# Optimization experiments

Hardware: AMD Instinct MI355X
Metric: run time of the kernel (lower is better)

The kernel has to match this reference:

```python
import jax, jax.numpy as jnp
import numpy as np

# loss weights from LineSegmentLoss.loss_w_dict (defaults)
W_TP_CENTER = 10.0

def smooth_l1(pred, gt):
    # F.smooth_l1_loss with default beta=1.0, reduction='none'
    d = jnp.abs(pred - gt)
    return jnp.where(d < 1.0, 0.5 * d * d, d - 0.5)

def bce_with_logits(logits, targets):
    # numerically stable BCE-with-logits, elementwise
    return jnp.maximum(logits, 0.0) - logits * targets + jnp.log1p(jnp.exp(-jnp.abs(logits)))

def weighted_bce_with_logits(out, gt, pos_w, neg_w):
    pos_mask = (gt != 0).astype(out.dtype)
    neg_mask = 1.0 - pos_mask
    loss = bce_with_logits(out, gt)
    loss_pos = (loss * pos_mask).sum() / pos_mask.sum()
    loss_neg = (loss * neg_mask).sum() / neg_mask.sum()
    return loss_pos * pos_w + loss_neg * neg_w

def displacement_loss_func(pred_dis, gt_dis):
    # pred_dis, gt_dis: [B, 4, H, W]
    pos_v = jnp.abs(gt_dis).sum(axis=1)                      # [B,H,W]
    pos_mask = (pos_v != 0).astype(pred_dis.dtype)           # [B,H,W]
    pos_mask_sum = pos_mask.sum()
    m = pos_mask[:, None, :, :]
    pred_m = pred_dis * m
    gt_m = gt_dis * m
    loss1 = smooth_l1(pred_m, gt_m).sum(axis=1)              # [B,H,W]
    # swap endpoints (x0,y0,x1,y1) -> (x1,y1,x0,y0)
    pred_swap = jnp.concatenate([pred_m[:, 2:], pred_m[:, :2]], axis=1)
    loss2 = smooth_l1(pred_swap, gt_m).sum(axis=1)
    return jnp.minimum(loss1, loss2).sum() / pos_mask_sum

def len_and_angle_loss_func(pred_len, pred_angle, gt_len, gt_angle):
    pred_len = jax.nn.sigmoid(pred_len)
    pred_angle = jax.nn.sigmoid(pred_angle)
    pos_mask = (gt_len != 0).astype(pred_len.dtype)
    pos_mask_sum = pos_mask.sum()
    len_loss = (smooth_l1(pred_len, gt_len) * pos_mask).sum() / pos_mask_sum
    angle_loss = (smooth_l1(pred_angle, gt_angle) * pos_mask).sum() / pos_mask_sum
    return len_loss, angle_loss

def setup_inputs() -> dict:
    key = jax.random.key(0)
    k1, k2, k3, k4, k5 = jax.random.split(key, 5)
    B, C, H, W = 32, 16, 256, 256
    preds = jax.random.normal(k1, (B, C, H, W), dtype=jnp.float32)
    base = jax.random.uniform(k2, (B, C, H, W), dtype=jnp.float32)
    keep = (jax.random.uniform(k3, (B, 1, H, W)) < 0.05).astype(jnp.float32)
    gts = base * keep
    tp_lines = jax.random.uniform(k4, (B, 64, 4), dtype=jnp.float32) * 512.0
    sol_lines = jax.random.uniform(k5, (B, 64, 4), dtype=jnp.float32) * 512.0
    return {"preds": preds, "gts": gts,
            "tp_gt_lines_512_list": tp_lines,
            "sol_gt_lines_512_list": sol_lines}

def reference(preds, gts, tp_gt_lines_512_list, sol_gt_lines_512_list):
    # line / junction segmentation losses (ch 15, 14)
    line_seg_loss = weighted_bce_with_logits(preds[:, 15], gts[:, 15], 1.0, 1.0)
    junc_seg_loss = weighted_bce_with_logits(preds[:, 14], gts[:, 14], 1.0, 30.0)
    # SOL block (ch 0..6)
    sol_center = weighted_bce_with_logits(preds[:, 0], gts[:, 0], 1.0, 30.0)
    sol_disp = displacement_loss_func(preds[:, 1:5], gts[:, 1:5])
    sol_len, sol_angle = len_and_angle_loss_func(preds[:, 5], preds[:, 6], gts[:, 5], gts[:, 6])
    # TP block (ch 7..13)
    tp_center = weighted_bce_with_logits(preds[:, 7], gts[:, 7], 1.0, 30.0)
    tp_disp = displacement_loss_func(preds[:, 8:12], gts[:, 8:12])
    tp_len, tp_angle = len_and_angle_loss_func(preds[:, 12], preds[:, 13], gts[:, 12], gts[:, 13])
    total = (W_TP_CENTER * tp_center + tp_disp + tp_len + tp_angle
             + sol_center + sol_disp + sol_len + sol_angle
             + line_seg_loss + junc_seg_loss)
    return total
```

## Files before the change

kernel.cpp:

```cpp
#include <hip/hip_runtime.h>
#include <math.h>

#define HW 65536
#define HW4 16384
#define CTOT 16
#define BATCH 32
#define NPIX (BATCH * HW)
#define NGRP (NPIX / 4)

#define NACC 22

__device__ __forceinline__ float smooth_l1(float p, float g) {
    float d = fabsf(p - g);
    return (d < 1.0f) ? 0.5f * d * d : d - 0.5f;
}
__device__ __forceinline__ float bce_logits(float x, float t) {
    return fmaxf(x, 0.0f) - x * t + log1pf(expf(-fabsf(x)));
}
__device__ __forceinline__ float sigmoidf_(float x) {
    return 1.0f / (1.0f + expf(-x));
}
__device__ __forceinline__ float get4(const float4& v, int j) {
    return j == 0 ? v.x : (j == 1 ? v.y : (j == 2 ? v.z : v.w));
}

__global__ __launch_bounds__(256) void loss_kernel(const float* __restrict__ preds,
                                                   const float* __restrict__ gts,
                                                   double* __restrict__ ws) {
    float acc[NACC];
#pragma unroll
    for (int i = 0; i < NACC; ++i) acc[i] = 0.0f;

    const int gtid = blockIdx.x * blockDim.x + threadIdx.x;
    const int stride = gridDim.x * blockDim.x;

    for (int g = gtid; g < NGRP; g += stride) {
        const int b   = g >> 14;
        const int hw4 = g & (HW4 - 1);
        const float4* pb = (const float4*)preds + (size_t)b * (CTOT * HW4) + hw4;
        const float4* gb = (const float4*)gts   + (size_t)b * (CTOT * HW4) + hw4;

        {
            const int ch[4]   = {15, 14, 0, 7};
            const int base[4] = {0, 3, 6, 9};
#pragma unroll
            for (int k = 0; k < 4; ++k) {
                float4 p = pb[(size_t)ch[k] * HW4];
                float4 t = gb[(size_t)ch[k] * HW4];
#pragma unroll
                for (int j = 0; j < 4; ++j) {
                    float x  = get4(p, j);
                    float tv = get4(t, j);
                    float loss = bce_logits(x, tv);
                    float pos  = (tv != 0.0f) ? 1.0f : 0.0f;
                    acc[base[k] + 0] += loss * pos;
                    acc[base[k] + 1] += loss * (1.0f - pos);
                    acc[base[k] + 2] += pos;
                }
            }
        }

        {
            const int c0[2]   = {1, 8};
            const int base[2] = {12, 14};
#pragma unroll
            for (int k = 0; k < 2; ++k) {
                float4 p0 = pb[(size_t)(c0[k] + 0) * HW4];
                float4 p1 = pb[(size_t)(c0[k] + 1) * HW4];
                float4 p2 = pb[(size_t)(c0[k] + 2) * HW4];
                float4 p3 = pb[(size_t)(c0[k] + 3) * HW4];
                float4 g0 = gb[(size_t)(c0[k] + 0) * HW4];
                float4 g1 = gb[(size_t)(c0[k] + 1) * HW4];
                float4 g2 = gb[(size_t)(c0[k] + 2) * HW4];
                float4 g3 = gb[(size_t)(c0[k] + 3) * HW4];
#pragma unroll
                for (int j = 0; j < 4; ++j) {
                    float a0 = get4(p0, j), a1 = get4(p1, j), a2 = get4(p2, j), a3 = get4(p3, j);
                    float b0 = get4(g0, j), b1 = get4(g1, j), b2 = get4(g2, j), b3 = get4(g3, j);
                    float posv = fabsf(b0) + fabsf(b1) + fabsf(b2) + fabsf(b3);
                    float m = (posv != 0.0f) ? 1.0f : 0.0f;
                    float l1 = smooth_l1(a0, b0) + smooth_l1(a1, b1) +
                               smooth_l1(a2, b2) + smooth_l1(a3, b3);
                    float l2 = smooth_l1(a2, b0) + smooth_l1(a3, b1) +
                               smooth_l1(a0, b2) + smooth_l1(a1, b3);
                    acc[base[k] + 0] += fminf(l1, l2) * m;
                    acc[base[k] + 1] += m;
                }
            }
        }

        {
            const int cl[2]   = {5, 12};
            const int base[2] = {16, 19};
#pragma unroll
            for (int k = 0; k < 2; ++k) {
                float4 pl = pb[(size_t)(cl[k] + 0) * HW4];
                float4 pa = pb[(size_t)(cl[k] + 1) * HW4];
                float4 gl = gb[(size_t)(cl[k] + 0) * HW4];
                float4 ga = gb[(size_t)(cl[k] + 1) * HW4];
#pragma unroll
                for (int j = 0; j < 4; ++j) {
                    float glv = get4(gl, j);
                    float m = (glv != 0.0f) ? 1.0f : 0.0f;
                    acc[base[k] + 0] += smooth_l1(sigmoidf_(get4(pl, j)), glv) * m;
                    acc[base[k] + 1] += smooth_l1(sigmoidf_(get4(pa, j)), get4(ga, j)) * m;
                    acc[base[k] + 2] += m;
                }
            }
        }
    }

#pragma unroll
    for (int i = 0; i < NACC; ++i) {
        float v = acc[i];
#pragma unroll
        for (int off = 32; off > 0; off >>= 1) v += __shfl_down(v, off, 64);
        acc[i] = v;
    }

    __shared__ float red[4][NACC];
    const int lane = threadIdx.x & 63;
    const int wid  = threadIdx.x >> 6;
    if (lane == 0) {
#pragma unroll
        for (int i = 0; i < NACC; ++i) red[wid][i] = acc[i];
    }
    __syncthreads();
    if (threadIdx.x < NACC) {
        float s = red[0][threadIdx.x] + red[1][threadIdx.x] +
                  red[2][threadIdx.x] + red[3][threadIdx.x];
        atomicAdd(&ws[threadIdx.x], (double)s);
    }
}

__global__ void finalize_kernel(const double* __restrict__ ws, float* __restrict__ out) {
    if (threadIdx.x == 0 && blockIdx.x == 0) {
        const double N = (double)NPIX;
        double line_seg   = ws[0] / ws[2]  +  1.0 * (ws[1]  / (N - ws[2]));
        double junc_seg   = ws[3] / ws[5]  + 30.0 * (ws[4]  / (N - ws[5]));
        double sol_center = ws[6] / ws[8]  + 30.0 * (ws[7]  / (N - ws[8]));
        double tp_center  = ws[9] / ws[11] + 30.0 * (ws[10] / (N - ws[11]));
        double sol_disp   = ws[12] / ws[13];
        double tp_disp    = ws[14] / ws[15];
        double sol_len    = ws[16] / ws[18];
        double sol_angle  = ws[17] / ws[18];
        double tp_len     = ws[19] / ws[21];
        double tp_angle   = ws[20] / ws[21];
        double total = 10.0 * tp_center + tp_disp + tp_len + tp_angle +
                       sol_center + sol_disp + sol_len + sol_angle +
                       line_seg + junc_seg;
        out[0] = (float)total;
    }
}

extern "C" void kernel_launch(void* const* d_in, const int* in_sizes, int n_in,
                              void* d_out, int out_size, void* d_ws, size_t ws_size,
                              hipStream_t stream) {
    const float* preds = (const float*)d_in[0];
    const float* gts   = (const float*)d_in[1];
    double* ws = (double*)d_ws;

    hipMemsetAsync(d_ws, 0, NACC * sizeof(double), stream);

    loss_kernel<<<1024, 256, 0, stream>>>(preds, gts, ws);
    finalize_kernel<<<1, 64, 0, stream>>>(ws, (float*)d_out);
}
```

Baseline: 297.4 us.

## Split loss kernel into per-task block ranges with fewer accumulators

Block indices are partitioned so each block handles a single loss term (BCE channel, displacement group, or len/angle pair) instead of every thread computing all 22 accumulators. This cuts register pressure and the reduction work per block, and doubles the grid to 2048 blocks. Load per block now varies: displacement blocks read 8 float4s per group while BCE blocks read 2, so block runtimes may be uneven and memory access is spread across different channel planes concurrently.

```diff
diff --git a/kernel.cpp b/kernel.cpp
--- a/kernel.cpp
+++ b/kernel.cpp
@@ -9,6 +9,8 @@
 #define NGRP (NPIX / 4)
 
 #define NACC 22
+
+#define GRID_BLOCKS 2048
 
 __device__ __forceinline__ float smooth_l1(float p, float g) {
     float d = fabsf(p - g);
@@ -27,109 +29,118 @@
 __global__ __launch_bounds__(256) void loss_kernel(const float* __restrict__ preds,
                                                    const float* __restrict__ gts,
                                                    double* __restrict__ ws) {
-    float acc[NACC];
+    const float4* pf = (const float4*)preds;
+    const float4* gf = (const float4*)gts;
+    const int blk = blockIdx.x;
+
+    float acc0 = 0.0f, acc1 = 0.0f, acc2 = 0.0f;
+    int base, nacc;
+
+    if (blk < 512) {
+        const int task = blk >> 7;
+        const int chs[4]   = {15, 14, 0, 7};
+        const int bases[4] = {0, 3, 6, 9};
+        const int ch = chs[task];
+        base = bases[task];
+        nacc = 3;
+        const int lthread = ((blk & 127) << 8) + threadIdx.x;
+        const int tstride = 128 * 256;
+#pragma unroll 2
+        for (int g = lthread; g < NGRP; g += tstride) {
+            const int b = g >> 14, hw4 = g & (HW4 - 1);
+            const size_t off = ((size_t)b * CTOT + ch) * HW4 + hw4;
+            float4 p = pf[off];
+            float4 t = gf[off];
 #pragma unroll
-    for (int i = 0; i < NACC; ++i) acc[i] = 0.0f;
-
-    const int gtid = blockIdx.x * blockDim.x + threadIdx.x;
-    const int stride = gridDim.x * blockDim.x;
-
-    for (int g = gtid; g < NGRP; g += stride) {
-        const int b   = g >> 14;
-        const int hw4 = g & (HW4 - 1);
-        const float4* pb = (const float4*)preds + (size_t)b * (CTOT * HW4) + hw4;
-        const float4* gb = (const float4*)gts   + (size_t)b * (CTOT * HW4) + hw4;
-
-        {
-            const int ch[4]   = {15, 14, 0, 7};
-            const int base[4] = {0, 3, 6, 9};
-#pragma unroll
-            for (int k = 0; k < 4; ++k) {
-                float4 p = pb[(size_t)ch[k] * HW4];
-                float4 t = gb[(size_t)ch[k] * HW4];
-#pragma unroll
-                for (int j = 0; j < 4; ++j) {
-                    float x  = get4(p, j);
-                    float tv = get4(t, j);
-                    float loss = bce_logits(x, tv);
-                    float pos  = (tv != 0.0f) ? 1.0f : 0.0f;
-                    acc[base[k] + 0] += loss * pos;
-                    acc[base[k] + 1] += loss * (1.0f - pos);
-                    acc[base[k] + 2] += pos;
-                }
+            for (int j = 0; j < 4; ++j) {
+                float x  = get4(p, j);
+                float tv = get4(t, j);
+                float loss = bce_logits(x, tv);
+                float pos  = (tv != 0.0f) ? 1.0f : 0.0f;
+                acc0 += loss * pos;
+                acc1 += loss * (1.0f - pos);
+                acc2 += pos;
             }
         }
-
-        {
-            const int c0[2]   = {1, 8};
-            const int base[2] = {12, 14};
+    } else if (blk < 1536) {
+        const int task = (blk - 512) >> 9;
+        const int c0 = task == 0 ? 1 : 8;
+        base = task == 0 ? 12 : 14;
+        nacc = 2;
+        const int lblk = (blk - 512) & 511;
+        const int lthread = (lblk << 8) + threadIdx.x;
+        const int tstride = 512 * 256;
+        for (int g = lthread; g < NGRP; g += tstride) {
+            const int b = g >> 14, hw4 = g & (HW4 - 1);
+            const size_t off = ((size_t)b * CTOT + c0) * HW4 + hw4;
+            float4 p0 = pf[off + 0 * HW4];
+            float4 p1 = pf[off + 1 * HW4];
+            float4 p2 = pf[off + 2 * HW4];
+            float4 p3 = pf[off + 3 * HW4];
+            float4 g0 = gf[off + 0 * HW4];
+            float4 g1 = gf[off + 1 * HW4];
+            float4 g2 = gf[off + 2 * HW4];
+            float4 g3 = gf[off + 3 * HW4];
 #pragma unroll
-            for (int k = 0; k < 2; ++k) {
-                float4 p0 = pb[(size_t)(c0[k] + 0) * HW4];
-                float4 p1 = pb[(size_t)(c0[k] + 1) * HW4];
-                float4 p2 = pb[(size_t)(c0[k] + 2) * HW4];
-                float4 p3 = pb[(size_t)(c0[k] + 3) * HW4];
-                float4 g0 = gb[(size_t)(c0[k] + 0) * HW4];
-                float4 g1 = gb[(size_t)(c0[k] + 1) * HW4];
-                float4 g2 = gb[(size_t)(c0[k] + 2) * HW4];
-                float4 g3 = gb[(size_t)(c0[k] + 3) * HW4];
-#pragma unroll
-                for (int j = 0; j < 4; ++j) {
-                    float a0 = get4(p0, j), a1 = get4(p1, j), a2 = get4(p2, j), a3 = get4(p3, j);
-                    float b0 = get4(g0, j), b1 = get4(g1, j), b2 = get4(g2, j), b3 = get4(g3, j);
-                    float posv = fabsf(b0) + fabsf(b1) + fabsf(b2) + fabsf(b3);
-                    float m = (posv != 0.0f) ? 1.0f : 0.0f;
-                    float l1 = smooth_l1(a0, b0) + smooth_l1(a1, b1) +
-                               smooth_l1(a2, b2) + smooth_l1(a3, b3);
-                    float l2 = smooth_l1(a2, b0) + smooth_l1(a3, b1) +
-                               smooth_l1(a0, b2) + smooth_l1(a1, b3);
-                    acc[base[k] + 0] += fminf(l1, l2) * m;
-                    acc[base[k] + 1] += m;
-                }
+            for (int j = 0; j < 4; ++j) {
+                float a0 = get4(p0, j), a1 = get4(p1, j), a2 = get4(p2, j), a3 = get4(p3, j);
+                float b0 = get4(g0, j), b1 = get4(g1, j), b2 = get4(g2, j), b3 = get4(g3, j);
+                float posv = fabsf(b0) + fabsf(b1) + fabsf(b2) + fabsf(b3);
+                float m = (posv != 0.0f) ? 1.0f : 0.0f;
+                float l1 = smooth_l1(a0, b0) + smooth_l1(a1, b1) +
+                           smooth_l1(a2, b2) + smooth_l1(a3, b3);
+                float l2 = smooth_l1(a2, b0) + smooth_l1(a3, b1) +
+                           smooth_l1(a0, b2) + smooth_l1(a1, b3);
+                acc0 += fminf(l1, l2) * m;
+                acc1 += m;
             }
         }
-
-        {
-            const int cl[2]   = {5, 12};
-            const int base[2] = {16, 19};
+    } else {
+        const int task = (blk - 1536) >> 8;
+        const int cl = task == 0 ? 5 : 12;
+        base = task == 0 ? 16 : 19;
+        nacc = 3;
+        const int lblk = (blk - 1536) & 255;
+        const int lthread = (lblk << 8) + threadIdx.x;
+        const int tstride = 256 * 256;
+#pragma unroll 2
+        for (int g = lthread; g < NGRP; g += tstride) {
+            const int b = g >> 14, hw4 = g & (HW4 - 1);
+            const size_t off = ((size_t)b * CTOT + cl) * HW4 + hw4;
+            float4 pl = pf[off + 0 * HW4];
+            float4 pa = pf[off + 1 * HW4];
+            float4 gl = gf[off + 0 * HW4];
+            float4 ga = gf[off + 1 * HW4];
 #pragma unroll
-            for (int k = 0; k < 2; ++k) {
-                float4 pl = pb[(size_t)(cl[k] + 0) * HW4];
-                float4 pa = pb[(size_t)(cl[k] + 1) * HW4];
-                float4 gl = gb[(size_t)(cl[k] + 0) * HW4];
-                float4 ga = gb[(size_t)(cl[k] + 1) * HW4];
-#pragma unroll
-                for (int j = 0; j < 4; ++j) {
-                    float glv = get4(gl, j);
-                    float m = (glv != 0.0f) ? 1.0f : 0.0f;
-                    acc[base[k] + 0] += smooth_l1(sigmoidf_(get4(pl, j)), glv) * m;
-                    acc[base[k] + 1] += smooth_l1(sigmoidf_(get4(pa, j)), get4(ga, j)) * m;
-                    acc[base[k] + 2] += m;
-                }
+            for (int j = 0; j < 4; ++j) {
+                float glv = get4(gl, j);
+                float m = (glv != 0.0f) ? 1.0f : 0.0f;
+                acc0 += smooth_l1(sigmoidf_(get4(pl, j)), glv) * m;
+                acc1 += smooth_l1(sigmoidf_(get4(pa, j)), get4(ga, j)) * m;
+                acc2 += m;
             }
         }
     }
 
 #pragma unroll
-    for (int i = 0; i < NACC; ++i) {
-        float v = acc[i];
-#pragma unroll
-        for (int off = 32; off > 0; off >>= 1) v += __shfl_down(v, off, 64);
-        acc[i] = v;
+    for (int off = 32; off > 0; off >>= 1) {
+        acc0 += __shfl_down(acc0, off, 64);
+        acc1 += __shfl_down(acc1, off, 64);
+        acc2 += __shfl_down(acc2, off, 64);
     }
 
-    __shared__ float red[4][NACC];
+    __shared__ float red[4][3];
     const int lane = threadIdx.x & 63;
     const int wid  = threadIdx.x >> 6;
-    if (lane == 0) {
-#pragma unroll
-        for (int i = 0; i < NACC; ++i) red[wid][i] = acc[i];
-    }
+    if (lane == 0) { red[wid][0] = acc0; red[wid][1] = acc1; red[wid][2] = acc2; }
     __syncthreads();
-    if (threadIdx.x < NACC) {
-        float s = red[0][threadIdx.x] + red[1][threadIdx.x] +
-                  red[2][threadIdx.x] + red[3][threadIdx.x];
-        atomicAdd(&ws[threadIdx.x], (double)s);
+    if (threadIdx.x == 0) {
+        float s0 = red[0][0] + red[1][0] + red[2][0] + red[3][0];
+        float s1 = red[0][1] + red[1][1] + red[2][1] + red[3][1];
+        float s2 = red[0][2] + red[1][2] + red[2][2] + red[3][2];
+        atomicAdd(&ws[base + 0], (double)s0);
+        atomicAdd(&ws[base + 1], (double)s1);
+        if (nacc == 3) atomicAdd(&ws[base + 2], (double)s2);
     }
 }
 
@@ -162,6 +173,6 @@
 
     hipMemsetAsync(d_ws, 0, NACC * sizeof(double), stream);
 
-    loss_kernel<<<1024, 256, 0, stream>>>(preds, gts, ws);
+    loss_kernel<<<GRID_BLOCKS, 256, 0, stream>>>(preds, gts, ws);
     finalize_kernel<<<1, 64, 0, stream>>>(ws, (float*)d_out);
 }
```

Measured after the change: 295.6 us. Within noise of the previous version (-0.6%).
